# Kernel optimization log

Measured on AMD Instinct MI355X. Metric: run time of the kernel, lower is better.

Reference implementation:

```python
import jax, jax.numpy as jnp
import numpy as np

N_JOINTS = 24

def _rodrigues(r):
    # r: [B, J, 3] axis-angle -> [B, J, 3, 3] rotation matrices
    theta = jnp.clip(jnp.linalg.norm(r, axis=-1, keepdims=True), 1e-6)  # [B,J,1]
    rh = r / theta
    z = jnp.zeros_like(rh[..., :1])
    # skew-symmetric matrix m
    m = jnp.stack([
        jnp.concatenate([z, -rh[..., 2:3], rh[..., 1:2]], -1),
        jnp.concatenate([rh[..., 2:3], z, -rh[..., 0:1]], -1),
        jnp.concatenate([-rh[..., 1:2], rh[..., 0:1], z], -1),
    ], axis=-2)  # [B,J,3,3]
    rrT = rh[..., :, None] * rh[..., None, :]  # outer product [B,J,3,3]
    cos = jnp.cos(theta)[..., None]
    sin = jnp.sin(theta)[..., None]
    eye = jnp.eye(3, dtype=r.dtype)
    return cos * eye + (1.0 - cos) * rrT + sin * m

def _with_zeros(Rm, t):
    # Rm: [B,3,3], t: [B,3] -> [B,4,4] homogeneous transform
    B = Rm.shape[0]
    top = jnp.concatenate([Rm, t[:, :, None]], axis=-1)  # [B,3,4]
    bot = jnp.broadcast_to(jnp.array([0.0, 0.0, 0.0, 1.0], Rm.dtype), (B, 1, 4))
    return jnp.concatenate([top, bot], axis=1)

def _keypoints(v, idx):
    # v: [B,N,3], idx: [G,K] vertex-index groups -> [B,G,3] via (max+min)/2
    g = v[:, idx]  # [B,G,K,3] irregular gather
    return (g.max(axis=2) + g.min(axis=2)) * 0.5

def setup_inputs() -> dict:
    key = jax.random.key(0)
    ks = jax.random.split(key, 8)
    B, N, P, K = 64, 40000, 100, 128
    beta = jax.random.normal(ks[0], (B, P), jnp.float32)
    pose = jax.random.normal(ks[1], (B, N_JOINTS * 3), jnp.float32) * 0.3
    trans = jax.random.normal(ks[2], (B, 3), jnp.float32)
    shapedirs = jax.random.normal(ks[3], (P, 3 * N), jnp.float32) * 0.01
    v_template = jax.random.normal(ks[4], (N, 3), jnp.float32)
    w = jax.random.uniform(ks[5], (N, N_JOINTS), jnp.float32)
    weights = w / w.sum(axis=1, keepdims=True)  # LBS weights sum to 1
    reorder_index = jnp.arange(N_JOINTS, dtype=jnp.int64 if jax.config.jax_enable_x64 else jnp.int32)
    # kinematic tree: parent[i] < i (binary-tree shape stands in for the rabbit skeleton)
    parent = jnp.concatenate([jnp.zeros(1, jnp.int32), (jnp.arange(1, N_JOINTS, dtype=jnp.int32) - 1) // 2])
    joint_idx = jax.random.randint(ks[6], (N_JOINTS - 1, K), 0, N)
    add_idx = jax.random.randint(ks[7], (7, K), 0, N)
    return {"beta": beta, "pose": pose, "trans": trans, "shapedirs": shapedirs,
            "v_template": v_template, "weights": weights, "reorder_index": reorder_index,
            "parent": parent, "joint_idx": joint_idx, "add_idx": add_idx}

def reference(beta, pose, trans, shapedirs, v_template, weights,
              reorder_index, parent, joint_idx, add_idx):
    B = beta.shape[0]
    pose = pose.reshape(B, N_JOINTS, 3)[:, reorder_index]
    # blend shapes: v_shaped = beta @ shapedirs + template
    v_posed = (beta @ shapedirs + v_template.reshape(-1)).reshape(B, -1, 3)  # [B,N,3]
    # joints from vertex-group (max+min)/2, root is zero
    J = jnp.concatenate([jnp.zeros((B, 1, 3), beta.dtype), _keypoints(v_posed, joint_idx)], axis=1)  # [B,24,3]
    R = _rodrigues(pose)  # [B,24,3,3]
    # forward kinematics along the tree (fixed 24-joint loop)
    par = np.asarray(jax.device_get(parent))
    G = [_with_zeros(R[:, 0], J[:, 0])]
    for i in range(1, N_JOINTS):
        p = int(par[i])
        G_loc = _with_zeros(R[:, i], J[:, i] - J[:, p])
        G.append(jnp.matmul(G[p], G_loc))
    G = jnp.stack(G, axis=1)  # [B,24,4,4]
    # remove rest-pose joint locations (pack subtraction only touches last column)
    Jh = jnp.concatenate([J, jnp.zeros((B, N_JOINTS, 1), beta.dtype)], axis=-1)[..., None]  # [B,24,4,1]
    t_corr = jnp.matmul(G, Jh)  # [B,24,4,1]
    G1 = jnp.concatenate([G[..., :3], G[..., 3:4] - t_corr], axis=-1)
    # LBS skinning: per-vertex blended transform
    T = jnp.einsum('nk,bkij->bnij', weights, G1)  # [B,N,4,4]
    vh = jnp.concatenate([v_posed, jnp.ones((B, v_posed.shape[1], 1), beta.dtype)], axis=-1)  # [B,N,4]
    posed = jnp.einsum('bnij,bnj->bni', T, vh)[..., :3] + trans[:, None, :]  # [B,N,3]
    skeleton = jnp.concatenate([
        jnp.zeros((B, 1, 3), beta.dtype),
        _keypoints(posed, joint_idx),
        _keypoints(posed, add_idx),
    ], axis=1)  # [B,31,3]
    return posed, skeleton
```

## Files before the change

### kernel.cpp

```cpp
#include <hip/hip_runtime.h>
#include <math.h>

#define B    64
#define NV   40000
#define P    100
#define KG   128
#define NJ   24
#define TVJ  16
#define TVS  32
#define NSK  31
#define NSUB (KG / TVJ)
#define NJS  (23 * NSUB)

typedef __attribute__((ext_vector_type(8))) short bf16x8;
typedef __attribute__((ext_vector_type(4))) float f32x4;

__device__ __forceinline__ unsigned short rne_bf16(float f) {
  unsigned u = __float_as_uint(f);
  u = (u + 0x7FFFu + ((u >> 16) & 1u)) >> 16;
  return (unsigned short)u;
}

__global__ __launch_bounds__(256)
void k_blend(const float* __restrict__ beta,
             const float* __restrict__ sd,
             const float* __restrict__ vt,
             float*       __restrict__ vp) {
  const int n0v  = blockIdx.x * TVS;
  const int col0 = n0v * 3;
  const int t  = threadIdx.x;
  const int lane = t & 63, wv = t >> 6;
  const int l15 = lane & 15, q = lane >> 4;

  __shared__ __align__(16) unsigned char smem[43904];
  unsigned short* beta_s = (unsigned short*)smem;
  unsigned short* sdT_s  = (unsigned short*)(smem + 17408);
  float*          vt_s   = (float*)(smem + 43520);
  float*          vhf2   = (float*)smem;

  for (int e = t; e < 64 * 36; e += 256) {
    const int m = e / 36, pp = P + e % 36;
    beta_s[m * 136 + pp] = 0;
  }
  for (int e = t; e < 64 * P; e += 256) {
    const int m = e / P, p = e % P;
    beta_s[m * 136 + p] = rne_bf16(beta[e]);
  }
  for (int task = t; task < 1536; task += 256) {
    const int n = task % 96, kg = task / 96;
    unsigned pk[4];
#pragma unroll
    for (int h = 0; h < 4; ++h) {
      const int k0 = kg * 8 + 2 * h;
      float f0 = 0.0f, f1 = 0.0f;
      if (k0 < P)     f0 = sd[(size_t)k0 * (3 * NV) + col0 + n];
      if (k0 + 1 < P) f1 = sd[(size_t)(k0 + 1) * (3 * NV) + col0 + n];
      pk[h] = (unsigned)rne_bf16(f0) | ((unsigned)rne_bf16(f1) << 16);
    }
    *(uint4*)&sdT_s[n * 136 + kg * 8] = make_uint4(pk[0], pk[1], pk[2], pk[3]);
  }
  if (t < 96) vt_s[t] = vt[col0 + t];
  __syncthreads();

  bf16x8 af[4];
#pragma unroll
  for (int ks = 0; ks < 4; ++ks)
    af[ks] = *(const bf16x8*)&beta_s[(wv * 16 + l15) * 136 + ks * 32 + q * 8];
  f32x4 acc[6];
#pragma unroll
  for (int nt = 0; nt < 6; ++nt) acc[nt] = (f32x4){0.f, 0.f, 0.f, 0.f};
#pragma unroll
  for (int ks = 0; ks < 4; ++ks) {
#pragma unroll
    for (int nt = 0; nt < 6; ++nt) {
      const bf16x8 bf = *(const bf16x8*)&sdT_s[(nt * 16 + l15) * 136 + ks * 32 + q * 8];
      acc[nt] = __builtin_amdgcn_mfma_f32_16x16x32_bf16(af[ks], bf, acc[nt], 0, 0, 0);
    }
  }
  __syncthreads();

#pragma unroll
  for (int nt = 0; nt < 6; ++nt) {
    const int n = nt * 16 + l15;
    const int v = n / 3, c = n - 3 * v;
    const float vtn = vt_s[n];
#pragma unroll
    for (int r = 0; r < 4; ++r) {
      const int m = wv * 16 + q * 4 + r;
      vhf2[v * 192 + m * 3 + c] = acc[nt][r] + vtn;
    }
  }
  __syncthreads();

  float* dst = vp + (size_t)n0v * 192;
  const float4* src = (const float4*)smem;
  for (int e = t; e < 1536; e += 256) ((float4*)dst)[e] = src[e];
}

__global__ __launch_bounds__(256)
void k_jkp(const float* __restrict__ vp,
           const int*   __restrict__ joint_idx,
           const float* __restrict__ pose,
           const float* __restrict__ trans,
           float*       __restrict__ pmn,
           float*       __restrict__ pmx,
           unsigned short* __restrict__ G1A,
           int*         __restrict__ cnt) {
  const int j = blockIdx.x;
  const int s = blockIdx.y;
  const int js = j * NSUB + s;
  const int t = threadIdx.x;

  __shared__ __align__(16) unsigned char smem[55296];
  float* pos_s = (float*)smem;
  __shared__ int idx_s[TVJ];
  __shared__ int s_old;

  if (t < TVJ) idx_s[t] = joint_idx[j * KG + s * TVJ + t];
  __syncthreads();

  for (int task = t; task < 768; task += 256) {
    const int r = task / 48, c4 = task % 48;
    const float4 v = *(const float4*)&vp[(size_t)idx_s[r] * 192 + c4 * 4];
    *(float4*)&pos_s[r * 192 + c4 * 4] = v;
  }
  __syncthreads();

  if (t < 192) {
    float lo = 1e30f, hi = -1e30f;
#pragma unroll
    for (int v = 0; v < TVJ; ++v) {
      const float val = pos_s[v * 192 + t];
      lo = fminf(lo, val); hi = fmaxf(hi, val);
    }
    pmn[js * 192 + t] = lo;
    pmx[js * 192 + t] = hi;
  }

  __syncthreads();
  if (t == 0) { __threadfence(); s_old = atomicAdd(cnt, 1); }
  __syncthreads();
  if (s_old != NJS - 1) return;
  __threadfence();

  float* Jl_c = (float*)smem;
  float* Gl   = (float*)(smem + 18432);

  {
    const uint4 z4 = make_uint4(0, 0, 0, 0);
    for (int e = t; e < 4096; e += 256) ((uint4*)G1A)[e] = z4;
  }
  for (int e = t; e < 192; e += 256) Jl_c[e] = 0.0f;
  for (int e = t; e < 23 * 192; e += 256) {
    const int jj = e / 192, rem = e - jj * 192;
    float lo = 1e30f, hi = -1e30f;
#pragma unroll
    for (int s2 = 0; s2 < NSUB; ++s2) {
      lo = fminf(lo, pmn[(jj * NSUB + s2) * 192 + rem]);
      hi = fmaxf(hi, pmx[(jj * NSUB + s2) * 192 + rem]);
    }
    const int b = rem / 3, c = rem - b * 3;
    Jl_c[((jj + 1) * 3 + c) * 64 + b] = 0.5f * (lo + hi);
  }
  __syncthreads();

  if (t < 64) {
    const int b = t;
    float px = pose[b * 72 + 0], py = pose[b * 72 + 1], pz = pose[b * 72 + 2];
    float G_[12];
#pragma unroll 1
    for (int i = 0; i < NJ; ++i) {
      float nx = 0.f, ny = 0.f, nz = 0.f;
      if (i < NJ - 1) {
        nx = pose[b * 72 + (i + 1) * 3 + 0];
        ny = pose[b * 72 + (i + 1) * 3 + 1];
        nz = pose[b * 72 + (i + 1) * 3 + 2];
      }
      const float th = fmaxf(sqrtf(px * px + py * py + pz * pz), 1e-6f);
      const float xh = px / th, yh = py / th, zh = pz / th;
      const float cc = cosf(th), ss = sinf(th), oo = 1.0f - cc;
      float R9[9];
      R9[0] = cc + oo * xh * xh;      R9[1] = oo * xh * yh - ss * zh; R9[2] = oo * xh * zh + ss * yh;
      R9[3] = oo * xh * yh + ss * zh; R9[4] = cc + oo * yh * yh;      R9[5] = oo * yh * zh - ss * xh;
      R9[6] = oo * xh * zh - ss * yh; R9[7] = oo * yh * zh + ss * xh; R9[8] = cc + oo * zh * zh;

      const float ji0 = Jl_c[(i * 3 + 0) * 64 + b];
      const float ji1 = Jl_c[(i * 3 + 1) * 64 + b];
      const float ji2 = Jl_c[(i * 3 + 2) * 64 + b];

      if (i == 0) {
#pragma unroll
        for (int r = 0; r < 3; ++r) {
          G_[r * 4 + 0] = R9[r * 3 + 0];
          G_[r * 4 + 1] = R9[r * 3 + 1];
          G_[r * 4 + 2] = R9[r * 3 + 2];
          G_[r * 4 + 3] = 0.0f;
        }
      } else {
        const int p = (i - 1) >> 1;
        const float d0 = ji0 - Jl_c[(p * 3 + 0) * 64 + b];
        const float d1 = ji1 - Jl_c[(p * 3 + 1) * 64 + b];
        const float d2 = ji2 - Jl_c[(p * 3 + 2) * 64 + b];
        float Gn[12];
#pragma unroll
        for (int r = 0; r < 3; ++r) {
          const float g0 = Gl[(b * 12 + p) * 12 + r * 4 + 0];
          const float g1 = Gl[(b * 12 + p) * 12 + r * 4 + 1];
          const float g2 = Gl[(b * 12 + p) * 12 + r * 4 + 2];
          const float g3 = Gl[(b * 12 + p) * 12 + r * 4 + 3];
          Gn[r * 4 + 0] = g0 * R9[0] + g1 * R9[3] + g2 * R9[6];
          Gn[r * 4 + 1] = g0 * R9[1] + g1 * R9[4] + g2 * R9[7];
          Gn[r * 4 + 2] = g0 * R9[2] + g1 * R9[5] + g2 * R9[8];
          Gn[r * 4 + 3] = g0 * d0 + g1 * d1 + g2 * d2 + g3;
        }
#pragma unroll
        for (int e = 0; e < 12; ++e) G_[e] = Gn[e];
      }
      if (i < 12) {
#pragma unroll
        for (int e = 0; e < 12; ++e) Gl[(b * 12 + i) * 12 + e] = G_[e];
      }
#pragma unroll
      for (int r = 0; r < 3; ++r) {
        const float tc = G_[r * 4 + 0] * ji0 + G_[r * 4 + 1] * ji1 + G_[r * 4 + 2] * ji2;
        G1A[b * 512 + (r * 4 + 0) * 32 + i] = rne_bf16(G_[r * 4 + 0]);
        G1A[b * 512 + (r * 4 + 1) * 32 + i] = rne_bf16(G_[r * 4 + 1]);
        G1A[b * 512 + (r * 4 + 2) * 32 + i] = rne_bf16(G_[r * 4 + 2]);
        G1A[b * 512 + (r * 4 + 3) * 32 + i] = rne_bf16(G_[r * 4 + 3] - tc);
      }
      px = nx; py = ny; pz = nz;
    }
  } else if (t >= 192) {
#pragma unroll
    for (int k = 0; k < 3; ++k) {
      const int e = (t - 192) * 3 + k;
      const int b = e / 3, r = e - b * 3;
      G1A[b * 512 + (r * 4 + 3) * 32 + 24] = rne_bf16(trans[b * 3 + r]);
    }
  }
}

__global__ __launch_bounds__(256)
void k_skin2(const float* __restrict__ vp,
             const float* __restrict__ w,
             const unsigned short* __restrict__ G1A,
             float*       __restrict__ out) {
  const int n0v  = blockIdx.x * TVS;
  const int col0 = n0v * 3;
  const int t  = threadIdx.x;
  const int lane = t & 63, wv = t >> 6;
  const int l15 = lane & 15, q = lane >> 4;

  __shared__ __align__(16) unsigned char smem[35328];
  float*          vhf  = (float*)smem;
  unsigned short* wT_s = (unsigned short*)(smem + 32768);

  for (int e = t; e < 1536; e += 256) {
    const int v = e / 48, j0 = (e % 48) * 4;
    const float4 f = *(const float4*)&vp[(size_t)(n0v + v) * 192 + j0];
    const float ff[4] = {f.x, f.y, f.z, f.w};
#pragma unroll
    for (int i = 0; i < 4; ++i) {
      const int jj = j0 + i;
      const int m = jj / 3, c = jj - 3 * m;
      vhf[m * 128 + v * 4 + c] = ff[i];
    }
  }
  for (int e = t; e < 1024; e += 256) {
    const int n = e >> 5, k = e & 31;
    float val = (k < NJ) ? w[(n0v + n) * NJ + k] : (k == NJ ? 1.0f : 0.0f);
    wT_s[n * 40 + k] = rne_bf16(val);
  }
  __syncthreads();

  const bf16x8 wf0 = *(const bf16x8*)&wT_s[l15 * 40 + q * 8];
  const bf16x8 wf1 = *(const bf16x8*)&wT_s[(16 + l15) * 40 + q * 8];
  const f32x4 zero = (f32x4){0.f, 0.f, 0.f, 0.f};
#pragma unroll 4
  for (int bi = 0; bi < 16; ++bi) {
    const int b = wv * 16 + bi;
    const bf16x8 gf = *(const bf16x8*)&G1A[(size_t)b * 512 + l15 * 32 + q * 8];
    const f32x4 d0 = __builtin_amdgcn_mfma_f32_16x16x32_bf16(gf, wf0, zero, 0, 0, 0);
    const f32x4 d1 = __builtin_amdgcn_mfma_f32_16x16x32_bf16(gf, wf1, zero, 0, 0, 0);
    const float4 vh0 = *(const float4*)&vhf[b * 128 + l15 * 4];
    const float4 vh1 = *(const float4*)&vhf[b * 128 + 64 + l15 * 4];
    if (q < 3) {
      out[(size_t)b * (NV * 3) + col0 + l15 * 3 + q] =
          d0[0] * vh0.x + d0[1] * vh0.y + d0[2] * vh0.z + d0[3];
      out[(size_t)b * (NV * 3) + col0 + 48 + l15 * 3 + q] =
          d1[0] * vh1.x + d1[1] * vh1.y + d1[2] * vh1.z + d1[3];
    }
  }
}

__global__ void k_skel(const float* __restrict__ posed,
                       const int*   __restrict__ joint_idx,
                       const int*   __restrict__ add_idx,
                       float*       __restrict__ skel) {
  const int j = blockIdx.x;
  const int b = blockIdx.y;
  const int t = threadIdx.x;
  const int idx = (j < 23) ? joint_idx[j * KG + t] : add_idx[(j - 23) * KG + t];

  const float* p = posed + (size_t)b * NV * 3 + (size_t)idx * 3;
  float mn[3], mx[3];
#pragma unroll
  for (int c = 0; c < 3; ++c) { mn[c] = p[c]; mx[c] = p[c]; }
#pragma unroll
  for (int off = 32; off > 0; off >>= 1) {
#pragma unroll
    for (int c = 0; c < 3; ++c) {
      mn[c] = fminf(mn[c], __shfl_down(mn[c], off));
      mx[c] = fmaxf(mx[c], __shfl_down(mx[c], off));
    }
  }
  __shared__ float s_mn[2][3], s_mx[2][3];
  const int wave = t >> 6, lane = t & 63;
  if (lane == 0) {
#pragma unroll
    for (int c = 0; c < 3; ++c) { s_mn[wave][c] = mn[c]; s_mx[wave][c] = mx[c]; }
  }
  __syncthreads();
  if (t == 0) {
#pragma unroll
    for (int c = 0; c < 3; ++c) {
      float lo = fminf(s_mn[0][c], s_mn[1][c]);
      float hi = fmaxf(s_mx[0][c], s_mx[1][c]);
      skel[(b * NSK + 1 + j) * 3 + c] = 0.5f * (lo + hi);
      if (j == 0) skel[(b * NSK + 0) * 3 + c] = 0.0f;
    }
  }
}

extern "C" void kernel_launch(void* const* d_in, const int* in_sizes, int n_in,
                              void* d_out, int out_size, void* d_ws, size_t ws_size,
                              hipStream_t stream) {
  const float* beta     = (const float*)d_in[0];
  const float* pose     = (const float*)d_in[1];
  const float* trans    = (const float*)d_in[2];
  const float* sd       = (const float*)d_in[3];
  const float* vt       = (const float*)d_in[4];
  const float* w        = (const float*)d_in[5];
  const int* joint_idx  = (const int*)d_in[8];
  const int* add_idx    = (const int*)d_in[9];

  float* out  = (float*)d_out;
  float* skel = out + (size_t)B * NV * 3;
  unsigned short* G1A = (unsigned short*)d_ws;
  float* pmn = (float*)((char*)d_ws + 65536);
  float* pmx = (float*)((char*)d_ws + 206848);
  int*   cnt = (int*)((char*)d_ws + 348160);
  float* vp  = (float*)((char*)d_ws + 348176);

  hipMemsetAsync(cnt, 0, 16, stream);
  k_blend<<<NV / TVS, 256, 0, stream>>>(beta, sd, vt, vp);
  k_jkp<<<dim3(23, NSUB), 256, 0, stream>>>(vp, joint_idx, pose, trans,
                                            pmn, pmx, G1A, cnt);
  k_skin2<<<NV / TVS, 256, 0, stream>>>(vp, w, G1A, out);
  k_skel<<<dim3(30, B), 128, 0, stream>>>(out, joint_idx, add_idx, skel);
}
```

Baseline: 183.3 us.

## Pad posed vertices to float4 layout, halve blend tile, fold memset into blend

Stores the shape-blended vertices padded to 4 floats per batch entry, so gathers in the joint kernel and loads in the skinning kernel become whole float4 copies without per-element scatter. The blend kernel now handles 16 vertices per block, doubling the grid and using less shared memory. It also zeroes the G1A buffer and the counter inside block 0, which drops the separate memset launch. The cost is a third more intermediate traffic from the padding, and the zeroing now relies on kernel ordering on the stream.

```diff
diff --git a/kernel.cpp b/kernel.cpp
--- a/kernel.cpp
+++ b/kernel.cpp
@@ -7,6 +7,7 @@
 #define KG   128
 #define NJ   24
 #define TVJ  16
+#define TVB  16
 #define TVS  32
 #define NSK  31
 #define NSUB (KG / TVJ)
@@ -25,18 +26,26 @@
 void k_blend(const float* __restrict__ beta,
              const float* __restrict__ sd,
              const float* __restrict__ vt,
-             float*       __restrict__ vp) {
-  const int n0v  = blockIdx.x * TVS;
+             float*       __restrict__ vp4,
+             unsigned short* __restrict__ G1A,
+             int*         __restrict__ cnt) {
+  const int n0v  = blockIdx.x * TVB;
   const int col0 = n0v * 3;
   const int t  = threadIdx.x;
   const int lane = t & 63, wv = t >> 6;
   const int l15 = lane & 15, q = lane >> 4;
 
-  __shared__ __align__(16) unsigned char smem[43904];
+  __shared__ __align__(16) unsigned char smem[30656];
   unsigned short* beta_s = (unsigned short*)smem;
   unsigned short* sdT_s  = (unsigned short*)(smem + 17408);
-  float*          vt_s   = (float*)(smem + 43520);
+  float*          vt_s   = (float*)(smem + 30464);
   float*          vhf2   = (float*)smem;
+
+  if (blockIdx.x == 0) {
+    const uint4 z4 = make_uint4(0, 0, 0, 0);
+    for (int e = t; e < 4096; e += 256) ((uint4*)G1A)[e] = z4;
+    if (t == 0) cnt[0] = 0;
+  }
 
   for (int e = t; e < 64 * 36; e += 256) {
     const int m = e / 36, pp = P + e % 36;
@@ -46,8 +55,8 @@
     const int m = e / P, p = e % P;
     beta_s[m * 136 + p] = rne_bf16(beta[e]);
   }
-  for (int task = t; task < 1536; task += 256) {
-    const int n = task % 96, kg = task / 96;
+  for (int task = t; task < 768; task += 256) {
+    const int n = task % 48, kg = task / 48;
     unsigned pk[4];
 #pragma unroll
     for (int h = 0; h < 4; ++h) {
@@ -59,46 +68,48 @@
     }
     *(uint4*)&sdT_s[n * 136 + kg * 8] = make_uint4(pk[0], pk[1], pk[2], pk[3]);
   }
-  if (t < 96) vt_s[t] = vt[col0 + t];
+  if (t < 48) vt_s[t] = vt[col0 + t];
   __syncthreads();
 
   bf16x8 af[4];
 #pragma unroll
   for (int ks = 0; ks < 4; ++ks)
     af[ks] = *(const bf16x8*)&beta_s[(wv * 16 + l15) * 136 + ks * 32 + q * 8];
-  f32x4 acc[6];
-#pragma unroll
-  for (int nt = 0; nt < 6; ++nt) acc[nt] = (f32x4){0.f, 0.f, 0.f, 0.f};
+  f32x4 acc[3];
+#pragma unroll
+  for (int nt = 0; nt < 3; ++nt) acc[nt] = (f32x4){0.f, 0.f, 0.f, 0.f};
 #pragma unroll
   for (int ks = 0; ks < 4; ++ks) {
 #pragma unroll
-    for (int nt = 0; nt < 6; ++nt) {
+    for (int nt = 0; nt < 3; ++nt) {
       const bf16x8 bf = *(const bf16x8*)&sdT_s[(nt * 16 + l15) * 136 + ks * 32 + q * 8];
       acc[nt] = __builtin_amdgcn_mfma_f32_16x16x32_bf16(af[ks], bf, acc[nt], 0, 0, 0);
     }
   }
-  __syncthreads();
-
-#pragma unroll
-  for (int nt = 0; nt < 6; ++nt) {
+  float vtv[3];
+#pragma unroll
+  for (int nt = 0; nt < 3; ++nt) vtv[nt] = vt_s[nt * 16 + l15];
+  __syncthreads();
+
+#pragma unroll
+  for (int nt = 0; nt < 3; ++nt) {
     const int n = nt * 16 + l15;
     const int v = n / 3, c = n - 3 * v;
-    const float vtn = vt_s[n];
 #pragma unroll
     for (int r = 0; r < 4; ++r) {
       const int m = wv * 16 + q * 4 + r;
-      vhf2[v * 192 + m * 3 + c] = acc[nt][r] + vtn;
-    }
-  }
-  __syncthreads();
-
-  float* dst = vp + (size_t)n0v * 192;
+      vhf2[v * 256 + m * 4 + c] = acc[nt][r] + vtv[nt];
+    }
+  }
+  __syncthreads();
+
+  float4* dst = (float4*)(vp4 + (size_t)n0v * 256);
   const float4* src = (const float4*)smem;
-  for (int e = t; e < 1536; e += 256) ((float4*)dst)[e] = src[e];
+  for (int e = t; e < 1024; e += 256) dst[e] = src[e];
 }
 
 __global__ __launch_bounds__(256)
-void k_jkp(const float* __restrict__ vp,
+void k_jkp(const float* __restrict__ vp4,
            const int*   __restrict__ joint_idx,
            const float* __restrict__ pose,
            const float* __restrict__ trans,
@@ -119,18 +130,20 @@
   if (t < TVJ) idx_s[t] = joint_idx[j * KG + s * TVJ + t];
   __syncthreads();
 
-  for (int task = t; task < 768; task += 256) {
-    const int r = task / 48, c4 = task % 48;
-    const float4 v = *(const float4*)&vp[(size_t)idx_s[r] * 192 + c4 * 4];
-    *(float4*)&pos_s[r * 192 + c4 * 4] = v;
+  {
+    float4* dst = (float4*)pos_s;
+    const float4* src = (const float4*)vp4;
+    for (int e = t; e < 1024; e += 256)
+      dst[e] = src[(size_t)idx_s[e >> 6] * 64 + (e & 63)];
   }
   __syncthreads();
 
   if (t < 192) {
+    const int b = t / 3, c = t - 3 * (t / 3);
     float lo = 1e30f, hi = -1e30f;
 #pragma unroll
     for (int v = 0; v < TVJ; ++v) {
-      const float val = pos_s[v * 192 + t];
+      const float val = pos_s[v * 256 + b * 4 + c];
       lo = fminf(lo, val); hi = fmaxf(hi, val);
     }
     pmn[js * 192 + t] = lo;
@@ -146,10 +159,6 @@
   float* Jl_c = (float*)smem;
   float* Gl   = (float*)(smem + 18432);
 
-  {
-    const uint4 z4 = make_uint4(0, 0, 0, 0);
-    for (int e = t; e < 4096; e += 256) ((uint4*)G1A)[e] = z4;
-  }
   for (int e = t; e < 192; e += 256) Jl_c[e] = 0.0f;
   for (int e = t; e < 23 * 192; e += 256) {
     const int jj = e / 192, rem = e - jj * 192;
@@ -241,7 +250,7 @@
 }
 
 __global__ __launch_bounds__(256)
-void k_skin2(const float* __restrict__ vp,
+void k_skin2(const float* __restrict__ vp4,
              const float* __restrict__ w,
              const unsigned short* __restrict__ G1A,
              float*       __restrict__ out) {
@@ -251,19 +260,15 @@
   const int lane = t & 63, wv = t >> 6;
   const int l15 = lane & 15, q = lane >> 4;
 
-  __shared__ __align__(16) unsigned char smem[35328];
-  float*          vhf  = (float*)smem;
-  unsigned short* wT_s = (unsigned short*)(smem + 32768);
-
-  for (int e = t; e < 1536; e += 256) {
-    const int v = e / 48, j0 = (e % 48) * 4;
-    const float4 f = *(const float4*)&vp[(size_t)(n0v + v) * 192 + j0];
-    const float ff[4] = {f.x, f.y, f.z, f.w};
-#pragma unroll
-    for (int i = 0; i < 4; ++i) {
-      const int jj = j0 + i;
-      const int m = jj / 3, c = jj - 3 * m;
-      vhf[m * 128 + v * 4 + c] = ff[i];
+  __shared__ __align__(16) unsigned char smem[35840];
+  float4*         vh4  = (float4*)smem;
+  unsigned short* wT_s = (unsigned short*)(smem + 33280);
+
+  {
+    const float4* src = (const float4*)(vp4 + (size_t)n0v * 256);
+    for (int i = t; i < 2048; i += 256) {
+      const int v = i >> 6, b = i & 63;
+      vh4[v * 65 + b] = src[i];
     }
   }
   for (int e = t; e < 1024; e += 256) {
@@ -282,8 +287,8 @@
     const bf16x8 gf = *(const bf16x8*)&G1A[(size_t)b * 512 + l15 * 32 + q * 8];
     const f32x4 d0 = __builtin_amdgcn_mfma_f32_16x16x32_bf16(gf, wf0, zero, 0, 0, 0);
     const f32x4 d1 = __builtin_amdgcn_mfma_f32_16x16x32_bf16(gf, wf1, zero, 0, 0, 0);
-    const float4 vh0 = *(const float4*)&vhf[b * 128 + l15 * 4];
-    const float4 vh1 = *(const float4*)&vhf[b * 128 + 64 + l15 * 4];
+    const float4 vh0 = vh4[l15 * 65 + b];
+    const float4 vh1 = vh4[(16 + l15) * 65 + b];
     if (q < 3) {
       out[(size_t)b * (NV * 3) + col0 + l15 * 3 + q] =
           d0[0] * vh0.x + d0[1] * vh0.y + d0[2] * vh0.z + d0[3];
@@ -350,12 +355,11 @@
   float* pmn = (float*)((char*)d_ws + 65536);
   float* pmx = (float*)((char*)d_ws + 206848);
   int*   cnt = (int*)((char*)d_ws + 348160);
-  float* vp  = (float*)((char*)d_ws + 348176);
-
-  hipMemsetAsync(cnt, 0, 16, stream);
-  k_blend<<<NV / TVS, 256, 0, stream>>>(beta, sd, vt, vp);
-  k_jkp<<<dim3(23, NSUB), 256, 0, stream>>>(vp, joint_idx, pose, trans,
+  float* vp4 = (float*)((char*)d_ws + 348176);
+
+  k_blend<<<NV / TVB, 256, 0, stream>>>(beta, sd, vt, vp4, G1A, cnt);
+  k_jkp<<<dim3(23, NSUB), 256, 0, stream>>>(vp4, joint_idx, pose, trans,
                                             pmn, pmx, G1A, cnt);
-  k_skin2<<<NV / TVS, 256, 0, stream>>>(vp, w, G1A, out);
+  k_skin2<<<NV / TVS, 256, 0, stream>>>(vp4, w, G1A, out);
   k_skel<<<dim3(30, B), 128, 0, stream>>>(out, joint_idx, add_idx, skel);
 }
```

Result: no change. 182.3 us (-0.5%).
